# Optimization experiments

Measured on AMD Instinct MI355X. Metric: run time of the kernel, lower is better.

Reference implementation:

```python
import jax, jax.numpy as jnp
import numpy as np

TRIAL_LEN = 1024   # embed dim (timesteps), = eqx MHA query_size
NUM_HEADS = 16
HEAD_DIM = TRIAL_LEN // NUM_HEADS  # 64, = RoPE embedding_size
SEQ = 2048         # hidden_size: number of spatial channels (sequence axis)
THETA = 10000.0


def _rope(x):
    # x: [S, H, D] -- equinox RotaryPositionalEmbedding (half-split convention),
    # identical for every head, so apply with broadcasting instead of vmap.
    S, _, D = x.shape
    half = D // 2
    freqs = 1.0 / (THETA ** (jnp.arange(half, dtype=jnp.float32) * 2.0 / D))  # [half]
    ang = jnp.arange(S, dtype=jnp.float32)[:, None] * freqs[None, :]          # [S, half]
    cos = jnp.cos(ang)[:, None, :]  # [S, 1, half]
    sin = jnp.sin(ang)[:, None, :]
    x1, x2 = jnp.split(x, 2, axis=-1)
    return jnp.concatenate([x1 * cos - x2 * sin, x2 * cos + x1 * sin], axis=-1)


def setup_inputs() -> dict:
    key = jax.random.key(0)
    ks = jax.random.split(key, 9)
    s = 1.0 / np.sqrt(TRIAL_LEN)
    f32 = jnp.float32
    return {
        "inputs": jax.random.normal(ks[0], (SEQ, TRIAL_LEN), f32),
        "Wq": jax.random.normal(ks[1], (TRIAL_LEN, TRIAL_LEN), f32) * s,
        "bq": jax.random.normal(ks[2], (TRIAL_LEN,), f32) * 0.01,
        "Wk": jax.random.normal(ks[3], (TRIAL_LEN, TRIAL_LEN), f32) * s,
        "bk": jax.random.normal(ks[4], (TRIAL_LEN,), f32) * 0.01,
        "Wv": jax.random.normal(ks[5], (TRIAL_LEN, TRIAL_LEN), f32) * s,
        "bv": jax.random.normal(ks[6], (TRIAL_LEN,), f32) * 0.01,
        "Wo": jax.random.normal(ks[7], (TRIAL_LEN, TRIAL_LEN), f32) * s,
        "bo": jax.random.normal(ks[8], (TRIAL_LEN,), f32) * 0.01,
    }


def reference(inputs, Wq, bq, Wk, bk, Wv, bv, Wo, bo):
    # QKV projections (eqx Linear: y = W @ x + b, weight [out, in])
    q = (inputs @ Wq.T + bq).reshape(SEQ, NUM_HEADS, HEAD_DIM)
    k = (inputs @ Wk.T + bk).reshape(SEQ, NUM_HEADS, HEAD_DIM)
    v = (inputs @ Wv.T + bv).reshape(SEQ, NUM_HEADS, HEAD_DIM)
    # process_heads: rotary embedding on query and key heads
    q = _rope(q)
    k = _rope(k)
    scale = jnp.float32(1.0 / np.sqrt(HEAD_DIM))
    logits = jnp.einsum("shd,thd->hst", q, k) * scale  # [H, S, S]
    attn = jax.nn.softmax(logits, axis=-1)
    o = jnp.einsum("hst,thd->shd", attn, v).reshape(SEQ, TRIAL_LEN)
    return o @ Wo.T + bo
```

## Files before the change

### kernel.cpp

```cpp
#include <hip/hip_runtime.h>
#include <cmath>

#define S_LEN 2048
#define EMB   1024
#define NH    16
#define HD    64
#define FIX_MAX 4.0f

typedef _Float16 half8 __attribute__((ext_vector_type(8)));
typedef _Float16 half4 __attribute__((ext_vector_type(4)));
typedef float    f32x4 __attribute__((ext_vector_type(4)));

__device__ __forceinline__ void gload_lds16(const _Float16* g, _Float16* l) {
    __builtin_amdgcn_global_load_lds(
        (const __attribute__((address_space(1))) void*)g,
        (__attribute__((address_space(3))) void*)l,
        16, 0, 0);
}

__device__ __forceinline__ void frag_unit_convert(
    const float* __restrict__ src, _Float16* __restrict__ dst, int unit, int lane)
{
    const int rb = unit >> 5, ks = unit & 31;
    const int row = lane & 15, quad = lane >> 4;
    const float* s = src + (size_t)(rb * 16 + row) * 1024 + ks * 32 + quad * 8;
    float4 a = *(const float4*)s;
    float4 b = *(const float4*)(s + 4);
    _Float16 h[8] = {(_Float16)a.x, (_Float16)a.y, (_Float16)a.z, (_Float16)a.w,
                     (_Float16)b.x, (_Float16)b.y, (_Float16)b.z, (_Float16)b.w};
    *(half8*)(dst + (size_t)unit * 512 + lane * 8) = *(half8*)h;
}

__global__ __launch_bounds__(256) void convert_all(
    const float* __restrict__ x,
    const float* __restrict__ Wq, const float* __restrict__ Wk,
    const float* __restrict__ Wv, const float* __restrict__ Wo,
    _Float16* __restrict__ xh,
    _Float16* __restrict__ whq, _Float16* __restrict__ whk,
    _Float16* __restrict__ whv, _Float16* __restrict__ who)
{
    const int tid = threadIdx.x;
    int u = blockIdx.x * 4 + (tid >> 6);
    const float* src; _Float16* dst; int unit;
    if (u < 4096) { src = x; dst = xh; unit = u; }
    else {
        const int w = (u - 4096) >> 11;
        unit = (u - 4096) & 2047;
        src = w == 0 ? Wq : w == 1 ? Wk : w == 2 ? Wv : Wo;
        dst = w == 0 ? whq : w == 1 ? whk : w == 2 ? whv : who;
    }
    frag_unit_convert(src, dst, unit, tid & 63);
}

__global__ __launch_bounds__(256) void qkv_gemm(
    const _Float16* __restrict__ xh,
    const _Float16* __restrict__ whq, const _Float16* __restrict__ whk,
    const _Float16* __restrict__ whv,
    const float* __restrict__ bq, const float* __restrict__ bk,
    const float* __restrict__ bv,
    _Float16* __restrict__ qh, _Float16* __restrict__ kh,
    _Float16* __restrict__ vT)
{
    const int z = blockIdx.y;
    const int b = blockIdx.x;
    const _Float16* Af = z == 0 ? whq : z == 1 ? whk : xh;
    const _Float16* Bf = z == 2 ? whv : xh;
    const float* bias  = z == 0 ? bq : z == 1 ? bk : bv;
    const int Atile = z < 2 ? (b >> 5) : (b >> 4);
    const int Btile = z < 2 ? (b & 31) : (b & 15);

    __shared__ __align__(16) _Float16 As[16 * 512];
    __shared__ __align__(16) _Float16 Bs[8 * 512];

    const int tid  = threadIdx.x;
    const int lane = tid & 63;
    const int wv   = tid >> 6;
    const int quad = lane >> 4;
    const int l16  = lane & 15;
    const int mb0  = Atile * 8;
    const int nb0  = Btile * 4;

    const int um0 = z < 2 ? ((wv >> 1) * 4 + (wv & 1)) : (wv * 2);
    const int um1 = z < 2 ? (um0 + 2) : (um0 + 1);

    f32x4 acc[2][4];
    #pragma unroll
    for (int m = 0; m < 2; ++m)
        #pragma unroll
        for (int n = 0; n < 4; ++n) acc[m][n] = (f32x4){0.f, 0.f, 0.f, 0.f};

    for (int ks0 = 0; ks0 < 32; ks0 += 2) {
        __syncthreads();
        #pragma unroll
        for (int i = 0; i < 4; ++i) {
            int u = wv * 4 + i;
            int ml = u >> 1, ksl = u & 1;
            gload_lds16(Af + ((size_t)(mb0 + ml) * 32 + ks0 + ksl) * 512 + lane * 8,
                        As + u * 512);
        }
        #pragma unroll
        for (int i = 0; i < 2; ++i) {
            int u = wv * 2 + i;
            int nl = u >> 1, ksl = u & 1;
            gload_lds16(Bf + ((size_t)(nb0 + nl) * 32 + ks0 + ksl) * 512 + lane * 8,
                        Bs + u * 512);
        }
        __syncthreads();

        #pragma unroll
        for (int ksl = 0; ksl < 2; ++ksl) {
            half8 a0 = *(const half8*)(As + (um0 * 2 + ksl) * 512 + lane * 8);
            half8 a1 = *(const half8*)(As + (um1 * 2 + ksl) * 512 + lane * 8);
            #pragma unroll
            for (int n = 0; n < 4; ++n) {
                half8 bb = *(const half8*)(Bs + (n * 2 + ksl) * 512 + lane * 8);
                acc[0][n] = __builtin_amdgcn_mfma_f32_16x16x32_f16(a0, bb, acc[0][n], 0, 0, 0);
                acc[1][n] = __builtin_amdgcn_mfma_f32_16x16x32_f16(a1, bb, acc[1][n], 0, 0, 0);
            }
        }
    }

    if (z == 2) {
        #pragma unroll
        for (int mu = 0; mu < 2; ++mu) {
            const int um  = wv * 2 + mu;
            const int t64 = Atile * 2 + (um >> 2);
            const int ts  = um & 3;
            #pragma unroll
            for (int n = 0; n < 4; ++n) {
                const int d  = Btile * 64 + n * 16 + l16;
                const float bvn = bias[d];
                _Float16 hv[4];
                #pragma unroll
                for (int r = 0; r < 4; ++r) hv[r] = (_Float16)(acc[mu][n][r] + bvn);
                _Float16* dst = vT + (((size_t)Btile * 32 + t64) * 16 + ts * 4 + n) * 256
                                 + lane * 4;
                *(half4*)dst = *(half4*)hv;
            }
        }
    } else {
        const int hh = Atile * 2 + (wv >> 1);
        const float qscale = z == 0 ? 0.125f : 1.0f;
        float fr[4], b0a[4], b1a[4];
        #pragma unroll
        for (int r = 0; r < 4; ++r) {
            const int i = (wv & 1) * 16 + quad * 4 + r;
            fr[r] = __expf(-(float)i * 0.2878231366242558f);
            const int d0 = Atile * 128 + um0 * 16 + quad * 4 + r;
            b0a[r] = bias[d0];
            b1a[r] = bias[d0 + 32];
        }
        const int quad_d = (wv & 1) * 2 + (quad >> 1);
        const int j0     = (quad & 1) * 4;
        _Float16* outp   = z == 0 ? qh : kh;
        #pragma unroll
        for (int n = 0; n < 4; ++n) {
            const int s  = Btile * 64 + n * 16 + l16;
            const int sb = Btile * 4 + n;
            _Float16 h1[4], h2[4];
            #pragma unroll
            for (int r = 0; r < 4; ++r) {
                const float ang = (float)s * fr[r];
                const float sn = sinf(ang), cs = cosf(ang);
                const float x1 = acc[0][n][r] + b0a[r];
                const float x2 = acc[1][n][r] + b1a[r];
                h1[r] = (_Float16)((x1 * cs - x2 * sn) * qscale);
                h2[r] = (_Float16)((x2 * cs + x1 * sn) * qscale);
            }
            _Float16* dst = outp + ((size_t)(hh * 128 + sb)) * 1024
                            + quad_d * 128 + l16 * 8 + j0;
            *(half4*)dst         = *(half4*)h1;
            *(half4*)(dst + 512) = *(half4*)h2;
        }
    }
}

__global__ __launch_bounds__(256) void gemm_out(
    const _Float16* __restrict__ Af, const _Float16* __restrict__ Bf,
    const float* __restrict__ bias, float* __restrict__ C)
{
    __shared__ __align__(16) _Float16 As[8 * 512];
    __shared__ __align__(16) _Float16 Bs[8 * 512];

    const int tid  = threadIdx.x;
    const int lane = tid & 63;
    const int wv   = tid >> 6;
    const int quad = lane >> 4;
    const int l16  = lane & 15;
    const int mb0  = blockIdx.y * 4;
    const int nb0  = blockIdx.x * 4;

    f32x4 acc[4];
    #pragma unroll
    for (int n = 0; n < 4; ++n) acc[n] = (f32x4){0.f, 0.f, 0.f, 0.f};

    for (int ks0 = 0; ks0 < 32; ks0 += 2) {
        __syncthreads();
        #pragma unroll
        for (int i = 0; i < 2; ++i) {
            gload_lds16(Af + ((size_t)(mb0 + wv) * 32 + ks0 + i) * 512 + lane * 8,
                        As + (wv * 2 + i) * 512);
            gload_lds16(Bf + ((size_t)(nb0 + wv) * 32 + ks0 + i) * 512 + lane * 8,
                        Bs + (wv * 2 + i) * 512);
        }
        __syncthreads();

        #pragma unroll
        for (int ksl = 0; ksl < 2; ++ksl) {
            half8 a = *(const half8*)(As + (wv * 2 + ksl) * 512 + lane * 8);
            #pragma unroll
            for (int n = 0; n < 4; ++n) {
                half8 b = *(const half8*)(Bs + (n * 2 + ksl) * 512 + lane * 8);
                acc[n] = __builtin_amdgcn_mfma_f32_16x16x32_f16(a, b, acc[n], 0, 0, 0);
            }
        }
    }

    #pragma unroll
    for (int n = 0; n < 4; ++n) {
        const int col = (nb0 + n) * 16 + l16;
        const float bv = bias[col];
        const int row = (mb0 + wv) * 16 + quad * 4;
        #pragma unroll
        for (int r = 0; r < 4; ++r)
            C[(size_t)(row + r) * 1024 + col] = acc[n][r] + bv;
    }
}

__global__ __launch_bounds__(256) void attn_mfma2(
    const _Float16* __restrict__ qh, const _Float16* __restrict__ kh,
    const _Float16* __restrict__ vT, _Float16* __restrict__ oh)
{
    __shared__ __align__(16) _Float16 Ks[8192];
    __shared__ __align__(16) _Float16 Vs[8192];

    const int tid  = threadIdx.x;
    const int lane = tid & 63;
    const int wv   = tid >> 6;
    const int quad = lane >> 4;
    const int l16  = lane & 15;
    const int h    = blockIdx.x & 15;
    const int rb   = (blockIdx.x >> 4) * 4 + wv;

    const _Float16* qbase = qh + ((size_t)h * 128 + rb) * 1024;
    half8 qf0 = *(const half8*)(qbase + lane * 8);
    half8 qf1 = *(const half8*)(qbase + 512 + lane * 8);

    f32x4 Of[4];
    #pragma unroll
    for (int d = 0; d < 4; ++d) Of[d] = (f32x4){0.f, 0.f, 0.f, 0.f};
    float l_acc = 0.f;

    for (int t0 = 0; t0 < S_LEN; t0 += 128) {
        __syncthreads();
        const _Float16* kg = kh + ((size_t)h * 128 + (t0 >> 4)) * 1024;
        const _Float16* vg = vT + ((size_t)h * 32  + (t0 >> 6)) * 4096;
        #pragma unroll
        for (int i = 0; i < 4; ++i) {
            gload_lds16(kg + (wv * 4 + i) * 512 + lane * 8, Ks + (wv * 4 + i) * 512);
            gload_lds16(vg + (wv * 4 + i) * 512 + lane * 8, Vs + (wv * 4 + i) * 512);
        }
        __syncthreads();

        #pragma unroll
        for (int ts = 0; ts < 8; ++ts) {
            half8 ka0 = *(const half8*)(Ks + ts * 1024 + lane * 8);
            half8 ka1 = *(const half8*)(Ks + ts * 1024 + 512 + lane * 8);
            f32x4 s = (f32x4){-FIX_MAX, -FIX_MAX, -FIX_MAX, -FIX_MAX};
            s = __builtin_amdgcn_mfma_f32_16x16x32_f16(ka0, qf0, s, 0, 0, 0);
            s = __builtin_amdgcn_mfma_f32_16x16x32_f16(ka1, qf1, s, 0, 0, 0);

            float p0 = __expf(s[0]), p1 = __expf(s[1]);
            float p2 = __expf(s[2]), p3 = __expf(s[3]);
            l_acc += (p0 + p1) + (p2 + p3);
            half4 pf = {(_Float16)p0, (_Float16)p1, (_Float16)p2, (_Float16)p3};

            #pragma unroll
            for (int db = 0; db < 4; ++db) {
                half4 va = *(const half4*)(Vs + (ts * 4 + db) * 256 + lane * 4);
                Of[db] = __builtin_amdgcn_mfma_f32_16x16x16f16(va, pf, Of[db], 0, 0, 0);
            }
        }
    }

    l_acc += __shfl_xor(l_acc, 16);
    l_acc += __shfl_xor(l_acc, 32);
    const float inv = 1.f / l_acc;

    #pragma unroll
    for (int db = 0; db < 4; ++db) {
        _Float16 hv[4];
        #pragma unroll
        for (int r = 0; r < 4; ++r) hv[r] = (_Float16)(Of[db][r] * inv);
        const int ks    = h * 2 + (db >> 1);
        const int quadk = (db & 1) * 2 + (quad >> 1);
        const int j0    = (quad & 1) * 4;
        _Float16* dst = oh + ((size_t)rb * 32 + ks) * 512 + quadk * 128 + l16 * 8 + j0;
        *(half4*)dst = *(half4*)hv;
    }
}

extern "C" void kernel_launch(void* const* d_in, const int* in_sizes, int n_in,
                              void* d_out, int out_size, void* d_ws, size_t ws_size,
                              hipStream_t stream) {
    const float* x  = (const float*)d_in[0];
    const float* Wq = (const float*)d_in[1];
    const float* bq = (const float*)d_in[2];
    const float* Wk = (const float*)d_in[3];
    const float* bk = (const float*)d_in[4];
    const float* Wv = (const float*)d_in[5];
    const float* bv = (const float*)d_in[6];
    const float* Wo = (const float*)d_in[7];
    const float* bo = (const float*)d_in[8];
    float* out = (float*)d_out;

    const size_t NELEM = (size_t)S_LEN * EMB;
    _Float16* hb = (_Float16*)d_ws;
    _Float16* xh  = hb;
    _Float16* qh  = xh + NELEM;
    _Float16* kh  = qh + NELEM;
    _Float16* vT  = kh + NELEM;
    _Float16* whq = vT + NELEM;
    _Float16* whk = whq + NELEM / 2;
    _Float16* whv = whk + NELEM / 2;
    _Float16* who = whv + NELEM / 2;
    _Float16* oh  = xh;

    convert_all<<<3072, 256, 0, stream>>>(x, Wq, Wk, Wv, Wo,
                                          xh, whq, whk, whv, who);

    qkv_gemm<<<dim3(256, 3), 256, 0, stream>>>(
        xh, whq, whk, whv, bq, bk, bv, qh, kh, vT);

    attn_mfma2<<<512, 256, 0, stream>>>(qh, kh, vT, oh);

    gemm_out<<<dim3(16, 32), 256, 0, stream>>>(oh, who, bo, out);
}
```

Before: 153.0 us.

## Fuse fp32-to-fp16 conversion into GEMM tile staging, drop convert kernel

Removes the separate conversion pass that wrote fp16 fragment-layout copies of the input and all four weight matrices. The QKV and output-projection GEMMs now load fp32 tiles directly, convert them in registers and store to LDS, replacing the async global-to-LDS copies. This saves one kernel launch and a full write and re-read of the converted tensors. In exchange each GEMM reads twice the bytes per tile, converts the same tiles repeatedly across blocks, and loses the direct-to-LDS load path.

```diff
diff --git a/kernel.cpp b/kernel.cpp
--- a/kernel.cpp
+++ b/kernel.cpp
@@ -18,44 +18,22 @@
         16, 0, 0);
 }
 
-__device__ __forceinline__ void frag_unit_convert(
-    const float* __restrict__ src, _Float16* __restrict__ dst, int unit, int lane)
+__device__ __forceinline__ void stage_unit_f32(
+    const float* __restrict__ src, int m, int ks, _Float16* lds_dst, int lane)
 {
-    const int rb = unit >> 5, ks = unit & 31;
     const int row = lane & 15, quad = lane >> 4;
-    const float* s = src + (size_t)(rb * 16 + row) * 1024 + ks * 32 + quad * 8;
+    const float* s = src + (size_t)(m * 16 + row) * 1024 + ks * 32 + quad * 8;
     float4 a = *(const float4*)s;
     float4 b = *(const float4*)(s + 4);
     _Float16 h[8] = {(_Float16)a.x, (_Float16)a.y, (_Float16)a.z, (_Float16)a.w,
                      (_Float16)b.x, (_Float16)b.y, (_Float16)b.z, (_Float16)b.w};
-    *(half8*)(dst + (size_t)unit * 512 + lane * 8) = *(half8*)h;
-}
-
-__global__ __launch_bounds__(256) void convert_all(
+    *(half8*)(lds_dst + lane * 8) = *(half8*)h;
+}
+
+__global__ __launch_bounds__(256) void qkv_gemm(
     const float* __restrict__ x,
     const float* __restrict__ Wq, const float* __restrict__ Wk,
-    const float* __restrict__ Wv, const float* __restrict__ Wo,
-    _Float16* __restrict__ xh,
-    _Float16* __restrict__ whq, _Float16* __restrict__ whk,
-    _Float16* __restrict__ whv, _Float16* __restrict__ who)
-{
-    const int tid = threadIdx.x;
-    int u = blockIdx.x * 4 + (tid >> 6);
-    const float* src; _Float16* dst; int unit;
-    if (u < 4096) { src = x; dst = xh; unit = u; }
-    else {
-        const int w = (u - 4096) >> 11;
-        unit = (u - 4096) & 2047;
-        src = w == 0 ? Wq : w == 1 ? Wk : w == 2 ? Wv : Wo;
-        dst = w == 0 ? whq : w == 1 ? whk : w == 2 ? whv : who;
-    }
-    frag_unit_convert(src, dst, unit, tid & 63);
-}
-
-__global__ __launch_bounds__(256) void qkv_gemm(
-    const _Float16* __restrict__ xh,
-    const _Float16* __restrict__ whq, const _Float16* __restrict__ whk,
-    const _Float16* __restrict__ whv,
+    const float* __restrict__ Wv,
     const float* __restrict__ bq, const float* __restrict__ bk,
     const float* __restrict__ bv,
     _Float16* __restrict__ qh, _Float16* __restrict__ kh,
@@ -63,9 +41,9 @@
 {
     const int z = blockIdx.y;
     const int b = blockIdx.x;
-    const _Float16* Af = z == 0 ? whq : z == 1 ? whk : xh;
-    const _Float16* Bf = z == 2 ? whv : xh;
-    const float* bias  = z == 0 ? bq : z == 1 ? bk : bv;
+    const float* Afp = z == 0 ? Wq : z == 1 ? Wk : x;
+    const float* Bfp = z == 2 ? Wv : x;
+    const float* bias = z == 0 ? bq : z == 1 ? bk : bv;
     const int Atile = z < 2 ? (b >> 5) : (b >> 4);
     const int Btile = z < 2 ? (b & 31) : (b & 15);
 
@@ -94,16 +72,12 @@
         #pragma unroll
         for (int i = 0; i < 4; ++i) {
             int u = wv * 4 + i;
-            int ml = u >> 1, ksl = u & 1;
-            gload_lds16(Af + ((size_t)(mb0 + ml) * 32 + ks0 + ksl) * 512 + lane * 8,
-                        As + u * 512);
+            stage_unit_f32(Afp, mb0 + (u >> 1), ks0 + (u & 1), As + u * 512, lane);
         }
         #pragma unroll
         for (int i = 0; i < 2; ++i) {
             int u = wv * 2 + i;
-            int nl = u >> 1, ksl = u & 1;
-            gload_lds16(Bf + ((size_t)(nb0 + nl) * 32 + ks0 + ksl) * 512 + lane * 8,
-                        Bs + u * 512);
+            stage_unit_f32(Bfp, nb0 + (u >> 1), ks0 + (u & 1), Bs + u * 512, lane);
         }
         __syncthreads();
 
@@ -176,7 +150,7 @@
 }
 
 __global__ __launch_bounds__(256) void gemm_out(
-    const _Float16* __restrict__ Af, const _Float16* __restrict__ Bf,
+    const _Float16* __restrict__ Af, const float* __restrict__ Wo,
     const float* __restrict__ bias, float* __restrict__ C)
 {
     __shared__ __align__(16) _Float16 As[8 * 512];
@@ -200,9 +174,10 @@
         for (int i = 0; i < 2; ++i) {
             gload_lds16(Af + ((size_t)(mb0 + wv) * 32 + ks0 + i) * 512 + lane * 8,
                         As + (wv * 2 + i) * 512);
-            gload_lds16(Bf + ((size_t)(nb0 + wv) * 32 + ks0 + i) * 512 + lane * 8,
-                        Bs + (wv * 2 + i) * 512);
-        }
+        }
+        #pragma unroll
+        for (int i = 0; i < 2; ++i)
+            stage_unit_f32(Wo, nb0 + wv, ks0 + i, Bs + (wv * 2 + i) * 512, lane);
         __syncthreads();
 
         #pragma unroll
@@ -316,23 +291,15 @@
 
     const size_t NELEM = (size_t)S_LEN * EMB;
     _Float16* hb = (_Float16*)d_ws;
-    _Float16* xh  = hb;
-    _Float16* qh  = xh + NELEM;
-    _Float16* kh  = qh + NELEM;
-    _Float16* vT  = kh + NELEM;
-    _Float16* whq = vT + NELEM;
-    _Float16* whk = whq + NELEM / 2;
-    _Float16* whv = whk + NELEM / 2;
-    _Float16* who = whv + NELEM / 2;
-    _Float16* oh  = xh;
-
-    convert_all<<<3072, 256, 0, stream>>>(x, Wq, Wk, Wv, Wo,
-                                          xh, whq, whk, whv, who);
+    _Float16* qh = hb;
+    _Float16* kh = qh + NELEM;
+    _Float16* vT = kh + NELEM;
+    _Float16* oh = vT + NELEM;
 
     qkv_gemm<<<dim3(256, 3), 256, 0, stream>>>(
-        xh, whq, whk, whv, bq, bk, bv, qh, kh, vT);
+        x, Wq, Wk, Wv, bq, bk, bv, qh, kh, vT);
 
     attn_mfma2<<<512, 256, 0, stream>>>(qh, kh, vT, oh);
 
-    gemm_out<<<dim3(16, 32), 256, 0, stream>>>(oh, who, bo, out);
-}
+    gemm_out<<<dim3(16, 32), 256, 0, stream>>>(oh, Wo, bo, out);
+}
```

Measured after the change: 204.6 us. +33.8%, slower.

## Fuse convert, QKV, attention and output GEMM into one persistent kernel with grid barriers

Applied to the files above, without the earlier changes.

Replaces four separate kernel launches with a single persistent kernel of 768 blocks that runs each phase in sequence, separated by atomic-counter grid barriers. Shared memory is reused across phases through one byte buffer, and the attention output gets its own workspace buffer instead of aliasing the converted input. This aims to remove launch and inter-kernel drain overhead. It relies on all 768 blocks being co-resident without a cooperative launch, and it adds barrier spin cost plus idle blocks in the later phases.

```diff
diff --git a/kernel.cpp b/kernel.cpp
--- a/kernel.cpp
+++ b/kernel.cpp
@@ -6,6 +6,7 @@
 #define NH    16
 #define HD    64
 #define FIX_MAX 4.0f
+#define NBLK  768
 
 typedef _Float16 half8 __attribute__((ext_vector_type(8)));
 typedef _Float16 half4 __attribute__((ext_vector_type(4)));
@@ -16,6 +17,19 @@
         (const __attribute__((address_space(1))) void*)g,
         (__attribute__((address_space(3))) void*)l,
         16, 0, 0);
+}
+
+__device__ __forceinline__ void grid_barrier(unsigned* ctr) {
+    __syncthreads();
+    if (threadIdx.x == 0) {
+        __threadfence();
+        __hip_atomic_fetch_add(ctr, 1u, __ATOMIC_RELAXED, __HIP_MEMORY_SCOPE_AGENT);
+        while (__hip_atomic_load(ctr, __ATOMIC_RELAXED, __HIP_MEMORY_SCOPE_AGENT)
+               < (unsigned)NBLK)
+            __builtin_amdgcn_s_sleep(2);
+        __threadfence();
+    }
+    __syncthreads();
 }
 
 __device__ __forceinline__ void frag_unit_convert(
@@ -31,28 +45,8 @@
     *(half8*)(dst + (size_t)unit * 512 + lane * 8) = *(half8*)h;
 }
 
-__global__ __launch_bounds__(256) void convert_all(
-    const float* __restrict__ x,
-    const float* __restrict__ Wq, const float* __restrict__ Wk,
-    const float* __restrict__ Wv, const float* __restrict__ Wo,
-    _Float16* __restrict__ xh,
-    _Float16* __restrict__ whq, _Float16* __restrict__ whk,
-    _Float16* __restrict__ whv, _Float16* __restrict__ who)
-{
-    const int tid = threadIdx.x;
-    int u = blockIdx.x * 4 + (tid >> 6);
-    const float* src; _Float16* dst; int unit;
-    if (u < 4096) { src = x; dst = xh; unit = u; }
-    else {
-        const int w = (u - 4096) >> 11;
-        unit = (u - 4096) & 2047;
-        src = w == 0 ? Wq : w == 1 ? Wk : w == 2 ? Wv : Wo;
-        dst = w == 0 ? whq : w == 1 ? whk : w == 2 ? whv : who;
-    }
-    frag_unit_convert(src, dst, unit, tid & 63);
-}
-
-__global__ __launch_bounds__(256) void qkv_gemm(
+__device__ __forceinline__ void qkv_tile(
+    int task, char* smem,
     const _Float16* __restrict__ xh,
     const _Float16* __restrict__ whq, const _Float16* __restrict__ whk,
     const _Float16* __restrict__ whv,
@@ -61,16 +55,16 @@
     _Float16* __restrict__ qh, _Float16* __restrict__ kh,
     _Float16* __restrict__ vT)
 {
-    const int z = blockIdx.y;
-    const int b = blockIdx.x;
+    const int z = task >> 8;
+    const int b = task & 255;
     const _Float16* Af = z == 0 ? whq : z == 1 ? whk : xh;
     const _Float16* Bf = z == 2 ? whv : xh;
     const float* bias  = z == 0 ? bq : z == 1 ? bk : bv;
     const int Atile = z < 2 ? (b >> 5) : (b >> 4);
     const int Btile = z < 2 ? (b & 31) : (b & 15);
 
-    __shared__ __align__(16) _Float16 As[16 * 512];
-    __shared__ __align__(16) _Float16 Bs[8 * 512];
+    _Float16* As = (_Float16*)smem;
+    _Float16* Bs = (_Float16*)(smem + 16384);
 
     const int tid  = threadIdx.x;
     const int lane = tid & 63;
@@ -175,72 +169,21 @@
     }
 }
 
-__global__ __launch_bounds__(256) void gemm_out(
-    const _Float16* __restrict__ Af, const _Float16* __restrict__ Bf,
-    const float* __restrict__ bias, float* __restrict__ C)
-{
-    __shared__ __align__(16) _Float16 As[8 * 512];
-    __shared__ __align__(16) _Float16 Bs[8 * 512];
+__device__ __forceinline__ void attn_tile(
+    int task, char* smem,
+    const _Float16* __restrict__ qh, const _Float16* __restrict__ kh,
+    const _Float16* __restrict__ vT, _Float16* __restrict__ oh)
+{
+    _Float16* Ks = (_Float16*)smem;
+    _Float16* Vs = (_Float16*)(smem + 16384);
 
     const int tid  = threadIdx.x;
     const int lane = tid & 63;
     const int wv   = tid >> 6;
     const int quad = lane >> 4;
     const int l16  = lane & 15;
-    const int mb0  = blockIdx.y * 4;
-    const int nb0  = blockIdx.x * 4;
-
-    f32x4 acc[4];
-    #pragma unroll
-    for (int n = 0; n < 4; ++n) acc[n] = (f32x4){0.f, 0.f, 0.f, 0.f};
-
-    for (int ks0 = 0; ks0 < 32; ks0 += 2) {
-        __syncthreads();
-        #pragma unroll
-        for (int i = 0; i < 2; ++i) {
-            gload_lds16(Af + ((size_t)(mb0 + wv) * 32 + ks0 + i) * 512 + lane * 8,
-                        As + (wv * 2 + i) * 512);
-            gload_lds16(Bf + ((size_t)(nb0 + wv) * 32 + ks0 + i) * 512 + lane * 8,
-                        Bs + (wv * 2 + i) * 512);
-        }
-        __syncthreads();
-
-        #pragma unroll
-        for (int ksl = 0; ksl < 2; ++ksl) {
-            half8 a = *(const half8*)(As + (wv * 2 + ksl) * 512 + lane * 8);
-            #pragma unroll
-            for (int n = 0; n < 4; ++n) {
-                half8 b = *(const half8*)(Bs + (n * 2 + ksl) * 512 + lane * 8);
-                acc[n] = __builtin_amdgcn_mfma_f32_16x16x32_f16(a, b, acc[n], 0, 0, 0);
-            }
-        }
-    }
-
-    #pragma unroll
-    for (int n = 0; n < 4; ++n) {
-        const int col = (nb0 + n) * 16 + l16;
-        const float bv = bias[col];
-        const int row = (mb0 + wv) * 16 + quad * 4;
-        #pragma unroll
-        for (int r = 0; r < 4; ++r)
-            C[(size_t)(row + r) * 1024 + col] = acc[n][r] + bv;
-    }
-}
-
-__global__ __launch_bounds__(256) void attn_mfma2(
-    const _Float16* __restrict__ qh, const _Float16* __restrict__ kh,
-    const _Float16* __restrict__ vT, _Float16* __restrict__ oh)
-{
-    __shared__ __align__(16) _Float16 Ks[8192];
-    __shared__ __align__(16) _Float16 Vs[8192];
-
-    const int tid  = threadIdx.x;
-    const int lane = tid & 63;
-    const int wv   = tid >> 6;
-    const int quad = lane >> 4;
-    const int l16  = lane & 15;
-    const int h    = blockIdx.x & 15;
-    const int rb   = (blockIdx.x >> 4) * 4 + wv;
+    const int h    = task & 15;
+    const int rb   = (task >> 4) * 4 + wv;
 
     const _Float16* qbase = qh + ((size_t)h * 128 + rb) * 1024;
     half8 qf0 = *(const half8*)(qbase + lane * 8);
@@ -298,6 +241,102 @@
         _Float16* dst = oh + ((size_t)rb * 32 + ks) * 512 + quadk * 128 + l16 * 8 + j0;
         *(half4*)dst = *(half4*)hv;
     }
+}
+
+__device__ __forceinline__ void out_tile(
+    int task, char* smem,
+    const _Float16* __restrict__ Af, const _Float16* __restrict__ Bf,
+    const float* __restrict__ bias, float* __restrict__ C)
+{
+    _Float16* As = (_Float16*)smem;
+    _Float16* Bs = (_Float16*)(smem + 8192);
+
+    const int tid  = threadIdx.x;
+    const int lane = tid & 63;
+    const int wv   = tid >> 6;
+    const int quad = lane >> 4;
+    const int l16  = lane & 15;
+    const int mb0  = (task >> 4) * 4;
+    const int nb0  = (task & 15) * 4;
+
+    f32x4 acc[4];
+    #pragma unroll
+    for (int n = 0; n < 4; ++n) acc[n] = (f32x4){0.f, 0.f, 0.f, 0.f};
+
+    for (int ks0 = 0; ks0 < 32; ks0 += 2) {
+        __syncthreads();
+        #pragma unroll
+        for (int i = 0; i < 2; ++i) {
+            gload_lds16(Af + ((size_t)(mb0 + wv) * 32 + ks0 + i) * 512 + lane * 8,
+                        As + (wv * 2 + i) * 512);
+            gload_lds16(Bf + ((size_t)(nb0 + wv) * 32 + ks0 + i) * 512 + lane * 8,
+                        Bs + (wv * 2 + i) * 512);
+        }
+        __syncthreads();
+
+        #pragma unroll
+        for (int ksl = 0; ksl < 2; ++ksl) {
+            half8 a = *(const half8*)(As + (wv * 2 + ksl) * 512 + lane * 8);
+            #pragma unroll
+            for (int n = 0; n < 4; ++n) {
+                half8 b = *(const half8*)(Bs + (n * 2 + ksl) * 512 + lane * 8);
+                acc[n] = __builtin_amdgcn_mfma_f32_16x16x32_f16(a, b, acc[n], 0, 0, 0);
+            }
+        }
+    }
+
+    #pragma unroll
+    for (int n = 0; n < 4; ++n) {
+        const int col = (nb0 + n) * 16 + l16;
+        const float bv = bias[col];
+        const int row = (mb0 + wv) * 16 + quad * 4;
+        #pragma unroll
+        for (int r = 0; r < 4; ++r)
+            C[(size_t)(row + r) * 1024 + col] = acc[n][r] + bv;
+    }
+}
+
+__global__ __launch_bounds__(256, 3) void mega(
+    const float* __restrict__ x,
+    const float* __restrict__ Wq, const float* __restrict__ bq,
+    const float* __restrict__ Wk, const float* __restrict__ bk,
+    const float* __restrict__ Wv, const float* __restrict__ bv,
+    const float* __restrict__ Wo, const float* __restrict__ bo,
+    float* __restrict__ out,
+    _Float16* __restrict__ xh, _Float16* __restrict__ qh,
+    _Float16* __restrict__ kh, _Float16* __restrict__ vT,
+    _Float16* __restrict__ whq, _Float16* __restrict__ whk,
+    _Float16* __restrict__ whv, _Float16* __restrict__ who,
+    _Float16* __restrict__ oh, unsigned* __restrict__ ctr)
+{
+    __shared__ __align__(16) char smem[32768];
+    const int tid = threadIdx.x;
+    const int bx  = blockIdx.x;
+
+    {
+        const int wgid = bx * 4 + (tid >> 6);
+        const int lane = tid & 63;
+        for (int u = wgid; u < 12288; u += 3072) {
+            const float* src; _Float16* dst; int unit;
+            if (u < 4096) { src = x; dst = xh; unit = u; }
+            else {
+                const int w = (u - 4096) >> 11;
+                unit = (u - 4096) & 2047;
+                src = w == 0 ? Wq : w == 1 ? Wk : w == 2 ? Wv : Wo;
+                dst = w == 0 ? whq : w == 1 ? whk : w == 2 ? whv : who;
+            }
+            frag_unit_convert(src, dst, unit, lane);
+        }
+    }
+    grid_barrier(ctr + 0);
+
+    qkv_tile(bx, smem, xh, whq, whk, whv, bq, bk, bv, qh, kh, vT);
+    grid_barrier(ctr + 16);
+
+    if (bx < 512) attn_tile(bx, smem, qh, kh, vT, oh);
+    grid_barrier(ctr + 32);
+
+    if (bx < 512) out_tile(bx, smem, oh, who, bo, out);
 }
 
 extern "C" void kernel_launch(void* const* d_in, const int* in_sizes, int n_in,
@@ -320,19 +359,17 @@
     _Float16* qh  = xh + NELEM;
     _Float16* kh  = qh + NELEM;
     _Float16* vT  = kh + NELEM;
-    _Float16* whq = vT + NELEM;
+    _Float16* oh  = vT + NELEM;
+    _Float16* whq = oh + NELEM;
     _Float16* whk = whq + NELEM / 2;
     _Float16* whv = whk + NELEM / 2;
     _Float16* who = whv + NELEM / 2;
-    _Float16* oh  = xh;
-
-    convert_all<<<3072, 256, 0, stream>>>(x, Wq, Wk, Wv, Wo,
-                                          xh, whq, whk, whv, who);
-
-    qkv_gemm<<<dim3(256, 3), 256, 0, stream>>>(
-        xh, whq, whk, whv, bq, bk, bv, qh, kh, vT);
-
-    attn_mfma2<<<512, 256, 0, stream>>>(qh, kh, vT, oh);
-
-    gemm_out<<<dim3(16, 32), 256, 0, stream>>>(oh, who, bo, out);
-}
+    unsigned* ctr = (unsigned*)((char*)d_ws + (48u << 20));
+
+    hipMemsetAsync(ctr, 0, 256, stream);
+
+    void* args_unused = nullptr; (void)args_unused;
+    mega<<<NBLK, 256, 0, stream>>>(
+        x, Wq, bq, Wk, bk, Wv, bv, Wo, bo, out,
+        xh, qh, kh, vT, whq, whk, whv, who, oh, ctr);
+}
```

Result: slower. 372.5 us (+143.6%).
